# Kernel optimization log

Hardware: AMD Instinct MI355X
Metric: run time of the kernel (lower is better)

## Reference

```python
import jax, jax.numpy as jnp
import numpy as np

WBITS = 2   # weight quantization bits (q_min_bits)
ABITS = 2   # activation quantization bits (out_bits, learnable since <=2)
SHIFT = 0   # activation pre-shift (config shift)


def quant_weight(w, bits=WBITS):
    """Symmetric per-tensor fake-quant with straight-through estimator."""
    qmax = 2.0 ** (bits - 1) - 1.0
    s = jnp.maximum(jnp.max(jnp.abs(w)) / qmax, 1e-8)
    q = jnp.round(w / s) * s
    return w + jax.lax.stop_gradient(q - w)


def quant_act(x, alpha, bits=ABITS, shift=SHIFT):
    """PACT-style learnable-clip activation fake-quant (unsigned, STE round)."""
    x = x * (2.0 ** (-shift))
    y = jnp.clip(x, 0.0, alpha)          # grad flows to alpha where clipped
    scale = alpha / (2.0 ** bits - 1.0)
    q = jnp.round(y / scale) * scale
    return y + jax.lax.stop_gradient(q - y)


def conv(x, w, pad):
    return jax.lax.conv_general_dilated(
        x, w, window_strides=(1, 1), padding=[(pad, pad), (pad, pad)],
        dimension_numbers=("NCHW", "OIHW", "NCHW"))


def maxpool2(x):
    return jax.lax.reduce_window(x, -jnp.inf, jax.lax.max,
                                 (1, 1, 2, 2), (1, 1, 2, 2), "VALID")


def setup_inputs() -> dict:
    key = jax.random.key(0)
    ks = jax.random.split(key, 5)
    B, H, W = 32, 224, 224
    x = jax.random.normal(ks[0], (B, 3, H, W), dtype=jnp.float32)
    # bits<=2 init branch: normal(mean=0, std=0.01)
    w1 = 0.01 * jax.random.normal(ks[1], (32, 3, 3, 3), dtype=jnp.float32)
    w2 = 0.01 * jax.random.normal(ks[2], (64, 32, 3, 3), dtype=jnp.float32)
    w3 = 0.01 * jax.random.normal(ks[3], (128, 64, 3, 3), dtype=jnp.float32)
    wc = 0.01 * jax.random.normal(ks[4], (10, 128, 1, 1), dtype=jnp.float32)
    a1 = jnp.ones((1,), jnp.float32)
    a2 = jnp.ones((1,), jnp.float32)
    a3 = jnp.ones((1,), jnp.float32)
    return {"x": x, "w1": w1, "w2": w2, "w3": w3, "wc": wc,
            "a1": a1, "a2": a2, "a3": a3}


def reference(x, w1, w2, w3, wc, a1, a2, a3):
    # block 1: QuantConv2d -> QuantizeActivation -> MaxPool2d(2)
    h = maxpool2(quant_act(conv(x, quant_weight(w1), 1), a1))
    # block 2
    h = maxpool2(quant_act(conv(h, quant_weight(w2), 1), a2))
    # block 3
    h = maxpool2(quant_act(conv(h, quant_weight(w3), 1), a3))
    # global amax pool over H, W (keepdim)
    h = jnp.max(h, axis=(2, 3), keepdims=True)
    # classifier: Dropout2d(eval=identity) + 1x1 QuantConv2d, no bias
    h = conv(h, quant_weight(wc), 0)
    return h.reshape(h.shape[0], -1)  # [B, num_classes]
```

## Files before the change

kernel.cpp:

```cpp
#include <hip/hip_runtime.h>
#include <math.h>


__global__ __launch_bounds__(64)
void prep_zero(unsigned* __restrict__ maxb) {
    if (threadIdx.x < 4) maxb[threadIdx.x] = 0u;
}

__global__ __launch_bounds__(256)
void prep_absmax(const float* __restrict__ w1, const float* __restrict__ w2,
                 const float* __restrict__ w3, const float* __restrict__ wc,
                 unsigned* __restrict__ maxb) {
    const float* srcs[4] = {w1, w2, w3, wc};
    const int    ns[4]   = {32*3*9, 64*32*9, 128*64*9, 10*128};
    const int t = blockIdx.y;
    const float* s = srcs[t];
    const int    N = ns[t];
    float m = 0.f;
    for (int i = blockIdx.x * 256 + threadIdx.x; i < N; i += 16 * 256)
        m = fmaxf(m, fabsf(s[i]));
    #pragma unroll
    for (int o = 32; o > 0; o >>= 1) m = fmaxf(m, __shfl_down(m, o));
    __shared__ float red[4];
    const int lane = threadIdx.x & 63, wid = threadIdx.x >> 6;
    if (lane == 0) red[wid] = m;
    __syncthreads();
    if (threadIdx.x == 0) {
        float mm = fmaxf(fmaxf(red[0], red[1]), fmaxf(red[2], red[3]));
        atomicMax(maxb + t, __float_as_uint(mm));
    }
}

__global__ __launch_bounds__(256)
void prep_qwc(const float* __restrict__ wc, const unsigned* __restrict__ maxb,
              float* __restrict__ qwc) {
    const float sc = fmaxf(__uint_as_float(maxb[3]), 1e-8f);
    const int i = blockIdx.x * 256 + threadIdx.x;
    if (i < 1280) qwc[i] = rintf(wc[i] / sc) * sc;
}

__global__ __launch_bounds__(256)
void build_lists(const float* __restrict__ w1, const float* __restrict__ w2,
                 const float* __restrict__ w3, const unsigned* __restrict__ maxb,
                 unsigned* __restrict__ h1, unsigned short* __restrict__ p1,
                 unsigned* __restrict__ h2, unsigned short* __restrict__ p2,
                 unsigned* __restrict__ h3, unsigned short* __restrict__ p3) {
    const float* wsrc[3] = {w1, w2, w3};
    unsigned*       hs[3] = {h1, h2, h3};
    unsigned short* ps[3] = {p1, p2, p3};
    const int cins[3] = {3, 32, 64};
    const int nch[3]  = {1, 8, 16};
    const int ngc[3]  = {2, 32, 128};
    const int t = blockIdx.y;
    const float* w = wsrc[t];
    const int CIN = cins[t], NCHUNK = nch[t];
    const int total = ngc[t] * 16;
    const float sc = fmaxf(__uint_as_float(maxb[t]), 1e-8f);
    for (int u = blockIdx.x * 256 + threadIdx.x; u < total; u += 8 * 256) {
        const int c = u & 15, rc = u >> 4;
        const int ch = rc % NCHUNK, grp = rc / NCHUNK;
        const int co = grp * 16 + c;
        unsigned* hdr = hs[t] + (size_t)rc * 36;
        unsigned short* inl = (unsigned short*)(hdr + 4);
        unsigned short* ovf = ps[t] + ((size_t)rc * 16 + c) * 32;
        int j = 0;
        for (int cil = 0; cil < 4; ++cil) {
            const int ci = ch * 4 + cil;
            if (ci >= CIN) break;
            for (int k = 0; k < 9; ++k) {
                const float q = rintf(w[(co * CIN + ci) * 9 + k] / sc);
                unsigned sgn;
                if (q > 0.5f)       sgn = 0u;
                else if (q < -0.5f) sgn = 0x8000u;
                else continue;
                const int kr = k / 3, kc = k % 3;
                const unsigned u0 =
                    (unsigned)(cil * 1360 + kr * 40 + 20 * (kc & 1) + (kc >> 1));
                const unsigned short e =
                    (unsigned short)(sgn | ((unsigned)(kc & 1) << 14) | u0);
                if (j < 4) inl[c * 4 + j] = e;
                else       ovf[j - 4] = e;
                ++j;
            }
        }
        ((unsigned char*)hdr)[c] = (unsigned char)j;
    }
}

#define APPLY_ENTRY(e)                                                     \
    {                                                                      \
        const float wv = ((e) & 0x8000u) ? sNeg : sPos;     \
        const float* pq0 = TB + ((e) & 0x3fffu);             \
        const float* pq1 = pq0 + (((e) & 0x4000u) ? -19 : 20);             \
        acc[c][0] = fmaf(wv, pq0[0],  acc[c][0]);                          \
        acc[c][1] = fmaf(wv, pq1[0],  acc[c][1]);                          \
        acc[c][2] = fmaf(wv, pq0[40], acc[c][2]);                          \
        acc[c][3] = fmaf(wv, pq1[40], acc[c][3]);                          \
    }

template<int CIN, int Co, int LIDX>
__global__ __launch_bounds__(256, 4)
void conv_sparse(const float* __restrict__ in, const unsigned* __restrict__ hdrs,
                 const unsigned short* __restrict__ pool,
                 const unsigned* __restrict__ maxb,
                 const float* __restrict__ alpha_p, float* __restrict__ out,
                 int H, int W) {
    constexpr int NCHUNK = (CIN + 3) / 4;
    constexpr int CCH    = (CIN < 4) ? CIN : 4;
    constexpr int NGRP   = Co / 16;
    const int PH = H >> 1, PW = W >> 1;
    const int tx = threadIdx.x, ty = threadIdx.y;
    const int tid = ty * 16 + tx;
    const int b   = blockIdx.z / NGRP;
    const int grp = blockIdx.z % NGRP;
    const int px  = blockIdx.x * 16 + tx;
    const int py  = blockIdx.y * 16 + ty;
    const int ix0 = blockIdx.x * 32 - 1;
    const int iy0 = blockIdx.y * 32 - 1;

    __shared__ float tile[CCH * 1360];
    const size_t HW = (size_t)H * W;
    const float* inB = in + (size_t)b * CIN * HW;

    int sidx[5], pofs[5];
    #pragma unroll
    for (int s = 0; s < 5; ++s) {
        const int idx = tid + 256 * s;
        const int r = idx / 34, c = idx - r * 34;
        const int gy = iy0 + r, gx = ix0 + c;
        sidx[s] = (idx < 1156 && gy >= 0 && gy < H && gx >= 0 && gx < W)
                  ? (gy * W + gx) : -1;
        pofs[s] = r * 40 + 20 * (c & 1) + (c >> 1);
    }

    float v[CCH][5];
    auto load_chunk = [&](int ch0) {
        #pragma unroll
        for (int ch = 0; ch < CCH; ++ch) {
            const float* inC = inB + (size_t)(ch0 + ch) * HW;
            #pragma unroll
            for (int s = 0; s < 5; ++s)
                v[ch][s] = (sidx[s] >= 0) ? inC[sidx[s]] : 0.f;
        }
    };
    auto store_tile = [&]() {
        #pragma unroll
        for (int ch = 0; ch < CCH; ++ch)
            #pragma unroll
            for (int s = 0; s < 5; ++s) {
                const int idx = tid + 256 * s;
                if (s < 4 || idx < 1156) tile[ch * 1360 + pofs[s]] = v[ch][s];
            }
    };

    const float sAbs = fmaxf(__uint_as_float(maxb[LIDX]), 1e-8f);
    const float sPos = __uint_as_float(__builtin_amdgcn_readfirstlane(__float_as_uint(sAbs)));
    const float sNeg = __uint_as_float(__builtin_amdgcn_readfirstlane(__float_as_uint(-sAbs)));

    float acc[16][4];
    #pragma unroll
    for (int c = 0; c < 16; ++c)
        #pragma unroll
        for (int q = 0; q < 4; ++q) acc[c][q] = 0.f;

    const float* TB = tile + (2 * ty) * 40 + tx;

    load_chunk(0);

    #pragma unroll 1
    for (int chunk = 0; chunk < NCHUNK; ++chunk) {
        const unsigned* hdr = hdrs + (size_t)(grp * NCHUNK + chunk) * 36;
        unsigned cntd[4];
        #pragma unroll
        for (int i = 0; i < 4; ++i) cntd[i] = hdr[i];
        unsigned ent[32];
        #pragma unroll
        for (int i = 0; i < 32; ++i) ent[i] = hdr[4 + i];

        __syncthreads();
        store_tile();
        if (chunk + 1 < NCHUNK) load_chunk((chunk + 1) * 4);
        __syncthreads();

        #pragma unroll
        for (int c = 0; c < 16; ++c) {
            const unsigned cnt = (cntd[c >> 2] >> ((c & 3) * 8)) & 0xffu;
            if (!cnt) continue;
            #pragma unroll
            for (int j = 0; j < 4; ++j) {
                if ((int)cnt > j) {
                    const unsigned e =
                        (ent[2 * c + (j >> 1)] >> ((j & 1) * 16)) & 0xffffu;
                    APPLY_ENTRY(e);
                }
            }
            if (cnt > 4) {
                const unsigned short* pp =
                    pool + ((size_t)(grp * NCHUNK + chunk) * 16 + c) * 32;
                #pragma unroll 1
                for (int j = 4; j < (int)cnt; ++j) {
                    const unsigned e = pp[j - 4];
                    APPLY_ENTRY(e);
                }
            }
        }
    }

    if (py < PH && px < PW) {
        const float alpha = *alpha_p;
        const float scale = alpha / 3.0f;
        #pragma unroll
        for (int c = 0; c < 16; ++c) {
            const float m = fmaxf(fmaxf(acc[c][0], acc[c][1]),
                                  fmaxf(acc[c][2], acc[c][3]));
            const float y = fminf(fmaxf(m, 0.f), alpha);
            out[(((size_t)b * Co + grp * 16 + c) * PH + py) * PW + px] =
                rintf(y / scale) * scale;
        }
    }
}

__global__ __launch_bounds__(64)
void gmax_kernel(const float* __restrict__ h3, float* __restrict__ g) {
    const int c = blockIdx.x, b = blockIdx.y;
    const float* p = h3 + ((size_t)b * 128 + c) * 784;
    float m = -INFINITY;
    for (int i = threadIdx.x; i < 784; i += 64) m = fmaxf(m, p[i]);
    #pragma unroll
    for (int o = 32; o > 0; o >>= 1) m = fmaxf(m, __shfl_down(m, o));
    if (threadIdx.x == 0) g[b * 128 + c] = m;
}

__global__ __launch_bounds__(128)
void classify_kernel(const float* __restrict__ g, const float* __restrict__ qwc,
                     float* __restrict__ out) {
    const int b = blockIdx.x;
    __shared__ float gg[128];
    gg[threadIdx.x] = g[b * 128 + threadIdx.x];
    __syncthreads();
    if (threadIdx.x < 10) {
        float s = 0.f;
        for (int k = 0; k < 128; ++k) s += qwc[threadIdx.x * 128 + k] * gg[k];
        out[b * 10 + threadIdx.x] = s;
    }
}

extern "C" void kernel_launch(void* const* d_in, const int* in_sizes, int n_in,
                              void* d_out, int out_size, void* d_ws, size_t ws_size,
                              hipStream_t stream) {
    const float* x  = (const float*)d_in[0];
    const float* w1 = (const float*)d_in[1];
    const float* w2 = (const float*)d_in[2];
    const float* w3 = (const float*)d_in[3];
    const float* wc = (const float*)d_in[4];
    const float* a1 = (const float*)d_in[5];
    const float* a2 = (const float*)d_in[6];
    const float* a3 = (const float*)d_in[7];

    float* ws = (float*)d_ws;
    size_t o = 0;
    float*    qwc  = ws + o; o += 1280;
    unsigned* maxb = (unsigned*)(ws + o); o += 4;
    float*    g    = ws + o; o += 32 * 128;
    unsigned*       h1 = (unsigned*)(ws + o);       o += 2   * 36;
    unsigned short* p1 = (unsigned short*)(ws + o); o += 2   * 16 * 16;
    unsigned*       h2 = (unsigned*)(ws + o);       o += 32  * 36;
    unsigned short* p2 = (unsigned short*)(ws + o); o += 32  * 16 * 16;
    unsigned*       h3 = (unsigned*)(ws + o);       o += 128 * 36;
    unsigned short* p3 = (unsigned short*)(ws + o); o += 128 * 16 * 16;
    float* h1p = ws + o; o += (size_t)32 * 32 * 112 * 112;
    float* h2p = ws + o; o += (size_t)32 * 64 * 56 * 56;
    float* h3p = ws + o; o += (size_t)32 * 128 * 28 * 28;

    prep_zero<<<1, 64, 0, stream>>>(maxb);
    prep_absmax<<<dim3(16, 4), 256, 0, stream>>>(w1, w2, w3, wc, maxb);
    prep_qwc<<<5, 256, 0, stream>>>(wc, maxb, qwc);
    build_lists<<<dim3(8, 3), 256, 0, stream>>>(w1, w2, w3, maxb,
                                                h1, p1, h2, p2, h3, p3);

    conv_sparse<3, 32, 0><<<dim3(7, 7, 32 * 2), dim3(16, 16), 0, stream>>>(
        x, h1, p1, maxb, a1, h1p, 224, 224);
    conv_sparse<32, 64, 1><<<dim3(4, 4, 32 * 4), dim3(16, 16), 0, stream>>>(
        h1p, h2, p2, maxb, a2, h2p, 112, 112);
    conv_sparse<64, 128, 2><<<dim3(2, 2, 32 * 8), dim3(16, 16), 0, stream>>>(
        h2p, h3, p3, maxb, a3, h3p, 56, 56);

    gmax_kernel<<<dim3(128, 32), 64, 0, stream>>>(h3p, g);
    classify_kernel<<<32, 128, 0, stream>>>(g, qwc, (float*)d_out);
}
```

Before: 258.2 us.

## Stage conv input tiles with direct global-to-LDS loads and double buffering

```diff
diff --git a/kernel.cpp b/kernel.cpp
--- a/kernel.cpp
+++ b/kernel.cpp
@@ -3,8 +3,9 @@
 
 
 __global__ __launch_bounds__(64)
-void prep_zero(unsigned* __restrict__ maxb) {
+void prep_zero(unsigned* __restrict__ maxb, float* __restrict__ zf) {
     if (threadIdx.x < 4) maxb[threadIdx.x] = 0u;
+    if (threadIdx.x == 4) *zf = 0.f;
 }
 
 __global__ __launch_bounds__(256)
@@ -75,7 +76,7 @@
                 else continue;
                 const int kr = k / 3, kc = k % 3;
                 const unsigned u0 =
-                    (unsigned)(cil * 1360 + kr * 40 + 20 * (kc & 1) + (kc >> 1));
+                    (unsigned)(cil * 1536 + kr * 40 + 20 * (kc & 1) + (kc >> 1));
                 const unsigned short e =
                     (unsigned short)(sgn | ((unsigned)(kc & 1) << 14) | u0);
                 if (j < 4) inl[c * 4 + j] = e;
@@ -103,14 +104,17 @@
 void conv_sparse(const float* __restrict__ in, const unsigned* __restrict__ hdrs,
                  const unsigned short* __restrict__ pool,
                  const unsigned* __restrict__ maxb,
-                 const float* __restrict__ alpha_p, float* __restrict__ out,
-                 int H, int W) {
+                 const float* __restrict__ alpha_p, const float* __restrict__ zf,
+                 float* __restrict__ out, int H, int W) {
     constexpr int NCHUNK = (CIN + 3) / 4;
     constexpr int CCH    = (CIN < 4) ? CIN : 4;
+    constexpr int NBUF   = (NCHUNK > 1) ? 2 : 1;
     constexpr int NGRP   = Co / 16;
+    constexpr int PLANE  = 1536;
     const int PH = H >> 1, PW = W >> 1;
     const int tx = threadIdx.x, ty = threadIdx.y;
     const int tid = ty * 16 + tx;
+    const int wbase = tid & ~63;
     const int b   = blockIdx.z / NGRP;
     const int grp = blockIdx.z % NGRP;
     const int px  = blockIdx.x * 16 + tx;
@@ -118,39 +122,45 @@
     const int ix0 = blockIdx.x * 32 - 1;
     const int iy0 = blockIdx.y * 32 - 1;
 
-    __shared__ float tile[CCH * 1360];
+    __shared__ float T[NBUF * CCH * PLANE];
     const size_t HW = (size_t)H * W;
     const float* inB = in + (size_t)b * CIN * HW;
 
-    int sidx[5], pofs[5];
+    const float* cur[6];
+    unsigned     step[6];
     #pragma unroll
-    for (int s = 0; s < 5; ++s) {
-        const int idx = tid + 256 * s;
-        const int r = idx / 34, c = idx - r * 34;
-        const int gy = iy0 + r, gx = ix0 + c;
-        sidx[s] = (idx < 1156 && gy >= 0 && gy < H && gx >= 0 && gx < W)
-                  ? (gy * W + gx) : -1;
-        pofs[s] = r * 40 + 20 * (c & 1) + (c >> 1);
-    }
-
-    float v[CCH][5];
-    auto load_chunk = [&](int ch0) {
+    for (int s = 0; s < 6; ++s) {
+        const int p = tid + 256 * s;
+        bool ok = false; int gidx = 0;
+        if (p < 1360) {
+            const int r = p / 40, q = p - r * 40;
+            int c = -1;
+            if (q < 17)                 c = 2 * q;
+            else if (q >= 20 && q < 37) c = 2 * (q - 20) + 1;
+            if (c >= 0) {
+                const int gy = iy0 + r, gx = ix0 + c;
+                if (gy >= 0 && gy < H && gx >= 0 && gx < W) {
+                    ok = true; gidx = gy * W + gx;
+                }
+            }
+        }
+        cur[s]  = ok ? (inB + gidx) : zf;
+        step[s] = ok ? (unsigned)HW : 0u;
+    }
+
+    auto stage = [&](int buf) {
         #pragma unroll
         for (int ch = 0; ch < CCH; ++ch) {
-            const float* inC = inB + (size_t)(ch0 + ch) * HW;
             #pragma unroll
-            for (int s = 0; s < 5; ++s)
-                v[ch][s] = (sidx[s] >= 0) ? inC[sidx[s]] : 0.f;
-        }
-    };
-    auto store_tile = [&]() {
-        #pragma unroll
-        for (int ch = 0; ch < CCH; ++ch)
+            for (int s = 0; s < 6; ++s)
+                __builtin_amdgcn_global_load_lds(
+                    (const __attribute__((address_space(1))) void*)cur[s],
+                    (__attribute__((address_space(3))) void*)
+                        &T[(buf * CCH + ch) * PLANE + s * 256 + wbase],
+                    4, 0, 0);
             #pragma unroll
-            for (int s = 0; s < 5; ++s) {
-                const int idx = tid + 256 * s;
-                if (s < 4 || idx < 1156) tile[ch * 1360 + pofs[s]] = v[ch][s];
-            }
+            for (int s = 0; s < 6; ++s) cur[s] += step[s];
+        }
     };
 
     const float sAbs = fmaxf(__uint_as_float(maxb[LIDX]), 1e-8f);
@@ -163,12 +173,11 @@
         #pragma unroll
         for (int q = 0; q < 4; ++q) acc[c][q] = 0.f;
 
-    const float* TB = tile + (2 * ty) * 40 + tx;
-
-    load_chunk(0);
+    stage(0);
 
     #pragma unroll 1
     for (int chunk = 0; chunk < NCHUNK; ++chunk) {
+        const int buf = chunk & (NBUF - 1);
         const unsigned* hdr = hdrs + (size_t)(grp * NCHUNK + chunk) * 36;
         unsigned cntd[4];
         #pragma unroll
@@ -178,9 +187,9 @@
         for (int i = 0; i < 32; ++i) ent[i] = hdr[4 + i];
 
         __syncthreads();
-        store_tile();
-        if (chunk + 1 < NCHUNK) load_chunk((chunk + 1) * 4);
-        __syncthreads();
+        if (chunk + 1 < NCHUNK) stage(buf ^ 1);
+
+        const float* TB = T + (buf * CCH) * PLANE + 80 * ty + tx;
 
         #pragma unroll
         for (int c = 0; c < 16; ++c) {
@@ -261,6 +270,7 @@
     size_t o = 0;
     float*    qwc  = ws + o; o += 1280;
     unsigned* maxb = (unsigned*)(ws + o); o += 4;
+    float*    zf   = ws + o; o += 4;
     float*    g    = ws + o; o += 32 * 128;
     unsigned*       h1 = (unsigned*)(ws + o);       o += 2   * 36;
     unsigned short* p1 = (unsigned short*)(ws + o); o += 2   * 16 * 16;
@@ -272,18 +282,18 @@
     float* h2p = ws + o; o += (size_t)32 * 64 * 56 * 56;
     float* h3p = ws + o; o += (size_t)32 * 128 * 28 * 28;
 
-    prep_zero<<<1, 64, 0, stream>>>(maxb);
+    prep_zero<<<1, 64, 0, stream>>>(maxb, zf);
     prep_absmax<<<dim3(16, 4), 256, 0, stream>>>(w1, w2, w3, wc, maxb);
     prep_qwc<<<5, 256, 0, stream>>>(wc, maxb, qwc);
     build_lists<<<dim3(8, 3), 256, 0, stream>>>(w1, w2, w3, maxb,
                                                 h1, p1, h2, p2, h3, p3);
 
     conv_sparse<3, 32, 0><<<dim3(7, 7, 32 * 2), dim3(16, 16), 0, stream>>>(
-        x, h1, p1, maxb, a1, h1p, 224, 224);
+        x, h1, p1, maxb, a1, zf, h1p, 224, 224);
     conv_sparse<32, 64, 1><<<dim3(4, 4, 32 * 4), dim3(16, 16), 0, stream>>>(
-        h1p, h2, p2, maxb, a2, h2p, 112, 112);
+        h1p, h2, p2, maxb, a2, zf, h2p, 112, 112);
     conv_sparse<64, 128, 2><<<dim3(2, 2, 32 * 8), dim3(16, 16), 0, stream>>>(
-        h2p, h3, p3, maxb, a3, h3p, 56, 56);
+        h2p, h3, p3, maxb, a3, zf, h3p, 56, 56);
 
     gmax_kernel<<<dim3(128, 32), 64, 0, stream>>>(h3p, g);
     classify_kernel<<<32, 128, 0, stream>>>(g, qwc, (float*)d_out);
```

Result: slower. 305.1 us (+18.2%).

## Split output channels across block halves with two pooled rows per thread

Applied to the files above, without the earlier changes.

```diff
diff --git a/kernel.cpp b/kernel.cpp
--- a/kernel.cpp
+++ b/kernel.cpp
@@ -75,7 +75,8 @@
                 else continue;
                 const int kr = k / 3, kc = k % 3;
                 const unsigned u0 =
-                    (unsigned)(cil * 1360 + kr * 40 + 20 * (kc & 1) + (kc >> 1));
+                    (unsigned)(cil * 1428 + kr * 42
+                               + ((kc & 1) ? 21 : 0) + (kc >> 1));
                 const unsigned short e =
                     (unsigned short)(sgn | ((unsigned)(kc & 1) << 14) | u0);
                 if (j < 4) inl[c * 4 + j] = e;
@@ -91,15 +92,19 @@
     {                                                                      \
         const float wv = ((e) & 0x8000u) ? sNeg : sPos;     \
         const float* pq0 = TB + ((e) & 0x3fffu);             \
-        const float* pq1 = pq0 + (((e) & 0x4000u) ? -19 : 20);             \
-        acc[c][0] = fmaf(wv, pq0[0],  acc[c][0]);                          \
-        acc[c][1] = fmaf(wv, pq1[0],  acc[c][1]);                          \
-        acc[c][2] = fmaf(wv, pq0[40], acc[c][2]);                          \
-        acc[c][3] = fmaf(wv, pq1[40], acc[c][3]);                          \
+        const float* pq1 = pq0 + (((e) & 0x4000u) ? -20 : 21);             \
+        acc[cl][0] = fmaf(wv, pq0[0],   acc[cl][0]);                       \
+        acc[cl][1] = fmaf(wv, pq1[0],   acc[cl][1]);                       \
+        acc[cl][2] = fmaf(wv, pq0[42],  acc[cl][2]);                       \
+        acc[cl][3] = fmaf(wv, pq1[42],  acc[cl][3]);                       \
+        acc[cl][4] = fmaf(wv, pq0[84],  acc[cl][4]);                       \
+        acc[cl][5] = fmaf(wv, pq1[84],  acc[cl][5]);                       \
+        acc[cl][6] = fmaf(wv, pq0[126], acc[cl][6]);                       \
+        acc[cl][7] = fmaf(wv, pq1[126], acc[cl][7]);                       \
     }
 
 template<int CIN, int Co, int LIDX>
-__global__ __launch_bounds__(256, 4)
+__global__ __launch_bounds__(256, 3)
 void conv_sparse(const float* __restrict__ in, const unsigned* __restrict__ hdrs,
                  const unsigned short* __restrict__ pool,
                  const unsigned* __restrict__ maxb,
@@ -108,17 +113,19 @@
     constexpr int NCHUNK = (CIN + 3) / 4;
     constexpr int CCH    = (CIN < 4) ? CIN : 4;
     constexpr int NGRP   = Co / 16;
+    constexpr int PLANE  = 1428;
     const int PH = H >> 1, PW = W >> 1;
     const int tx = threadIdx.x, ty = threadIdx.y;
+    const int tyy = ty & 7, half = ty >> 3;
     const int tid = ty * 16 + tx;
     const int b   = blockIdx.z / NGRP;
     const int grp = blockIdx.z % NGRP;
     const int px  = blockIdx.x * 16 + tx;
-    const int py  = blockIdx.y * 16 + ty;
+    const int py0 = blockIdx.y * 16 + 2 * tyy;
     const int ix0 = blockIdx.x * 32 - 1;
     const int iy0 = blockIdx.y * 32 - 1;
 
-    __shared__ float tile[CCH * 1360];
+    __shared__ float tile[CCH * PLANE];
     const size_t HW = (size_t)H * W;
     const float* inB = in + (size_t)b * CIN * HW;
 
@@ -130,7 +137,7 @@
         const int gy = iy0 + r, gx = ix0 + c;
         sidx[s] = (idx < 1156 && gy >= 0 && gy < H && gx >= 0 && gx < W)
                   ? (gy * W + gx) : -1;
-        pofs[s] = r * 40 + 20 * (c & 1) + (c >> 1);
+        pofs[s] = r * 42 + ((c & 1) ? 21 : 0) + (c >> 1);
     }
 
     float v[CCH][5];
@@ -149,7 +156,8 @@
             #pragma unroll
             for (int s = 0; s < 5; ++s) {
                 const int idx = tid + 256 * s;
-                if (s < 4 || idx < 1156) tile[ch * 1360 + pofs[s]] = v[ch][s];
+                if (s < 4 || idx < 1156)
+                    tile[ch * PLANE + pofs[s]] = v[ch][s];
             }
     };
 
@@ -157,25 +165,25 @@
     const float sPos = __uint_as_float(__builtin_amdgcn_readfirstlane(__float_as_uint(sAbs)));
     const float sNeg = __uint_as_float(__builtin_amdgcn_readfirstlane(__float_as_uint(-sAbs)));
 
-    float acc[16][4];
+    float acc[8][8];
     #pragma unroll
-    for (int c = 0; c < 16; ++c)
-        #pragma unroll
-        for (int q = 0; q < 4; ++q) acc[c][q] = 0.f;
-
-    const float* TB = tile + (2 * ty) * 40 + tx;
+    for (int cl = 0; cl < 8; ++cl)
+        #pragma unroll
+        for (int q = 0; q < 8; ++q) acc[cl][q] = 0.f;
+
+    const float* TB = tile + 168 * tyy + tx;
 
     load_chunk(0);
 
     #pragma unroll 1
     for (int chunk = 0; chunk < NCHUNK; ++chunk) {
         const unsigned* hdr = hdrs + (size_t)(grp * NCHUNK + chunk) * 36;
-        unsigned cntd[4];
-        #pragma unroll
-        for (int i = 0; i < 4; ++i) cntd[i] = hdr[i];
-        unsigned ent[32];
-        #pragma unroll
-        for (int i = 0; i < 32; ++i) ent[i] = hdr[4 + i];
+        unsigned cntd[2];
+        #pragma unroll
+        for (int i = 0; i < 2; ++i) cntd[i] = hdr[2 * half + i];
+        unsigned ent[16];
+        #pragma unroll
+        for (int i = 0; i < 16; ++i) ent[i] = hdr[4 + 16 * half + i];
 
         __syncthreads();
         store_tile();
@@ -183,20 +191,21 @@
         __syncthreads();
 
         #pragma unroll
-        for (int c = 0; c < 16; ++c) {
-            const unsigned cnt = (cntd[c >> 2] >> ((c & 3) * 8)) & 0xffu;
+        for (int cl = 0; cl < 8; ++cl) {
+            const unsigned cnt = (cntd[cl >> 2] >> ((cl & 3) * 8)) & 0xffu;
             if (!cnt) continue;
             #pragma unroll
             for (int j = 0; j < 4; ++j) {
                 if ((int)cnt > j) {
                     const unsigned e =
-                        (ent[2 * c + (j >> 1)] >> ((j & 1) * 16)) & 0xffffu;
+                        (ent[2 * cl + (j >> 1)] >> ((j & 1) * 16)) & 0xffffu;
                     APPLY_ENTRY(e);
                 }
             }
             if (cnt > 4) {
                 const unsigned short* pp =
-                    pool + ((size_t)(grp * NCHUNK + chunk) * 16 + c) * 32;
+                    pool + ((size_t)(grp * NCHUNK + chunk) * 16
+                            + 8 * half + cl) * 32;
                 #pragma unroll 1
                 for (int j = 4; j < (int)cnt; ++j) {
                     const unsigned e = pp[j - 4];
@@ -206,16 +215,24 @@
         }
     }
 
-    if (py < PH && px < PW) {
+    if (px < PW) {
         const float alpha = *alpha_p;
         const float scale = alpha / 3.0f;
         #pragma unroll
-        for (int c = 0; c < 16; ++c) {
-            const float m = fmaxf(fmaxf(acc[c][0], acc[c][1]),
-                                  fmaxf(acc[c][2], acc[c][3]));
-            const float y = fminf(fmaxf(m, 0.f), alpha);
-            out[(((size_t)b * Co + grp * 16 + c) * PH + py) * PW + px] =
-                rintf(y / scale) * scale;
+        for (int cl = 0; cl < 8; ++cl) {
+            float* ob = out + ((size_t)b * Co + grp * 16 + half * 8 + cl)
+                              * PH * PW;
+            #pragma unroll
+            for (int j = 0; j < 2; ++j) {
+                const int py = py0 + j;
+                if (py < PH) {
+                    const float m =
+                        fmaxf(fmaxf(acc[cl][4*j+0], acc[cl][4*j+1]),
+                              fmaxf(acc[cl][4*j+2], acc[cl][4*j+3]));
+                    const float y = fminf(fmaxf(m, 0.f), alpha);
+                    ob[(size_t)py * PW + px] = rintf(y / scale) * scale;
+                }
+            }
         }
     }
 }
```

After: 299.5 us. +16.0%, slower.
